# Kernel optimization log

Measured on AMD Instinct MI355X. Metric: run time of the kernel, lower is better.

The kernel has to match this reference:

```python
import jax, jax.numpy as jnp
import numpy as np

C = 64
K = 16
DEPTH = 4            # int(sqrt(K))
N_NODES = K - 1      # 15 internal nodes per subspace tree
D = 512              # input feature dim, D // C = 8 per subspace
M = 512              # output dim (LUT rows)
N = 16384            # number of input rows


def _make_selection_matrix(C, depth=DEPTH):
    # row i within a subspace selects the transformed dim used at tree level of node i
    lvl = [0, 1, 1, 2, 2, 2, 2, 3, 3, 3, 3, 3, 3, 3, 3]
    S = np.zeros((C * N_NODES, C * depth), np.float32)
    for c in range(C):
        for i in range(N_NODES):
            S[c * N_NODES + i, c * depth + lvl[i]] = 1.0
    return S


def _make_bit_matrix(C, K=K):
    # per-subspace (K, K-1) matrix: leaf k gets +/-1 on the 4 nodes along its root-to-leaf path
    Bm = np.zeros((K, N_NODES), np.float32)
    for k in range(K):
        node = 0
        for l in range(DEPTH):
            bit = (k >> (DEPTH - 1 - l)) & 1
            Bm[k, node] = 1.0 if bit else -1.0
            node = 2 * node + 1 + bit  # children of node i are 2i+1 (left) and 2i+2 (right)
    Bfull = np.zeros((C * K, C * N_NODES), np.float32)
    for c in range(C):
        Bfull[c * K:(c + 1) * K, c * N_NODES:(c + 1) * N_NODES] = Bm
    return Bfull


def setup_inputs() -> dict:
    key = jax.random.key(0)
    k1, k2, k3, k4 = jax.random.split(key, 4)
    I = jax.random.normal(k1, (N, D), dtype=jnp.float32)
    A = jax.random.normal(k2, (C, D // C, DEPTH), dtype=jnp.float32) * (1.0 / np.sqrt(D // C))
    T = jax.random.normal(k3, (C * N_NODES,), dtype=jnp.float32) * 0.1
    L = jax.random.normal(k4, (M, C, K), dtype=jnp.float32)
    S = jnp.asarray(_make_selection_matrix(C))
    B = jnp.asarray(_make_bit_matrix(C))
    return {"I": I, "A": A, "T": T, "L": L, "S": S, "B": B}


def reference(I, A, T, L, S, B):
    C_, sub, depth = A.shape
    Kq = L.shape[-1]
    n = I.shape[0]
    # block-diagonal per-subspace projection: (n, D) -> (n, C*depth)
    Ir = I.T.reshape(C_, sub, n)                      # (C, sub, n)
    xt = jnp.einsum('csn,csd->cdn', Ir, A)            # (C, depth, n)
    xt = xt.reshape(C_ * depth, n)                    # (C*depth, n)
    # tree encoding: per-node activations, tanh relaxation, leaf scores
    h = S @ xt - T[:, None]                           # (C*15, n)
    b = (B @ jnp.tanh(h)).reshape(C_, Kq, n)          # (C, K, n)
    # straight-through hard one-hot encoding with softmax backward
    E_soft = jax.nn.softmax(b, axis=1)
    E_hard = jax.nn.one_hot(jnp.argmax(b, axis=1), Kq, axis=1, dtype=b.dtype)
    E = E_hard + E_soft - jax.lax.stop_gradient(E_soft)  # (C, K, n)
    # LUT decode: out[n, m] = sum_c L[m, c, enc(n, c)]
    out = jnp.einsum('mck,ckn->nm', L, E)
    return out
```

## Files before the change

kernel.cpp:

```cpp
#include <hip/hip_runtime.h>
#include <hip/hip_fp16.h>
#include <math.h>

#define CC 64
#define KK 16
#define NNODES 15
#define DD 512
#define MM 512
#define NN 16384

typedef _Float16 half8 __attribute__((ext_vector_type(8)));
typedef float f32x4 __attribute__((ext_vector_type(4)));
typedef unsigned long long u64;

__device__ __forceinline__ float xla_tanhf(float x) {
    const float kMax = 7.90531110763549805f;
    bool tiny = fabsf(x) < 0.0004f;
    float xc = fminf(fmaxf(x, -kMax), kMax);
    float x2 = __fmul_rn(xc, xc);
    float p = __fmaf_rn(x2, -2.76076847742355e-16f, 2.00018790482477e-13f);
    p = __fmaf_rn(x2, p, -8.60467152213735e-11f);
    p = __fmaf_rn(x2, p, 5.12229709037114e-08f);
    p = __fmaf_rn(x2, p, 1.48572235717979e-05f);
    p = __fmaf_rn(x2, p, 6.37261928875436e-04f);
    p = __fmaf_rn(x2, p, 4.89352455891786e-03f);
    p = __fmul_rn(xc, p);
    float q = __fmaf_rn(x2, 1.19825839466702e-06f, 1.18534705686654e-04f);
    q = __fmaf_rn(x2, q, 2.26843463243900e-03f);
    q = __fmaf_rn(x2, q, 4.89352518554385e-03f);
    return tiny ? x : __fdiv_rn(p, q);
}

__global__ __launch_bounds__(256) void pack_bfrag(const float* __restrict__ L,
                                                  uint4* __restrict__ Bpk) {
    const int t    = blockIdx.x * 256 + threadIdx.x;
    const int lane = t & 63;
    const int mtg  = (t >> 6) & 31;
    const int ks   = t >> 11;
    const int kbase = ks * 32 + ((lane >> 4) << 3);
    const int c     = kbase >> 4;
    const int slot0 = kbase & 15;
    const int m     = (mtg << 4) + (lane & 15);

    const float* src = L + ((size_t)m * CC + c) * KK + slot0;
    float4 v0 = ((const float4*)src)[0];
    float4 v1 = ((const float4*)src)[1];
    union { half8 h; uint4 u; } pk;
    pk.h[0] = (_Float16)v0.x; pk.h[1] = (_Float16)v0.y;
    pk.h[2] = (_Float16)v0.z; pk.h[3] = (_Float16)v0.w;
    pk.h[4] = (_Float16)v1.x; pk.h[5] = (_Float16)v1.y;
    pk.h[6] = (_Float16)v1.z; pk.h[7] = (_Float16)v1.w;
    Bpk[t] = pk.u;
}

__global__ __launch_bounds__(256, 4) void encode_kernel(const float* __restrict__ I,
                                                        const float* __restrict__ A,
                                                        const float* __restrict__ T,
                                                        unsigned* __restrict__ codesG) {
    __shared__ float sA[32 * 64];
    __shared__ float sT[CC * NNODES];

    const int tid = threadIdx.x;
    for (int i = tid; i < CC * 32; i += 256) sA[(i & 31) * 64 + (i >> 5)] = A[i];
    for (int i = tid; i < CC * NNODES; i += 256) sT[i] = T[i];
    __syncthreads();

    const int lane = tid & 63;
    const int c    = lane;
    const int w    = ((blockIdx.x & 3) << 2) + (tid >> 6);
    const int tile = blockIdx.x >> 2;
    const int n0   = tile * 64;

    float a_[32];
#pragma unroll
    for (int i = 0; i < 32; ++i) a_[i] = sA[i * 64 + c];
    float tt[NNODES];
#pragma unroll
    for (int i = 0; i < NNODES; ++i) tt[i] = sT[c * NNODES + i];

    const int lvl[NNODES] = {0, 1, 1, 2, 2, 2, 2, 3, 3, 3, 3, 3, 3, 3, 3};
    unsigned codeWord = 0;
#pragma unroll 2
    for (int rr = 0; rr < 4; ++rr) {
        const int rl = (rr << 4) + w;
        const float* Ij = I + (size_t)(n0 + rl) * DD + c * 8;
        float4 v0 = ((const float4*)Ij)[0];
        float4 v1 = ((const float4*)Ij)[1];
        float iv[8] = {v0.x, v0.y, v0.z, v0.w, v1.x, v1.y, v1.z, v1.w};

        float t[4] = {0.f, 0.f, 0.f, 0.f};
#pragma unroll
        for (int s = 0; s < 8; ++s) {
            float v = iv[s];
#pragma unroll
            for (int d = 0; d < 4; ++d)
                t[d] = __fmaf_rn(v, a_[(s << 2) + d], t[d]);
        }

        float th[NNODES];
#pragma unroll
        for (int i = 0; i < NNODES; ++i) {
            float h = __fsub_rn(t[lvl[i]], tt[i]);
            th[i] = xla_tanhf(h);
        }

        int best = 0;
        float bestv = -3.0e38f;
#pragma unroll
        for (int k = 0; k < KK; ++k) {
            int node = 0;
            float s = 0.f;
#pragma unroll
            for (int l = 0; l < 4; ++l) {
                int bit = (k >> (3 - l)) & 1;
                s = __fadd_rn(s, bit ? th[node] : -th[node]);
                node = 2 * node + 1 + bit;
            }
            if (s > bestv) { bestv = s; best = k; }
        }
        codeWord |= ((unsigned)best) << (rr << 3);
    }
    codesG[(size_t)tile * 1024 + (w << 6) + c] = codeWord;
}

__global__ __launch_bounds__(256, 4) void decode_kernel(const unsigned* __restrict__ codesG,
                                                        const uint4* __restrict__ Bpk,
                                                        float* __restrict__ out) {
    __shared__ unsigned sCodes[16 * 68];

    const int tid  = threadIdx.x;
    const int tile = blockIdx.x >> 2;
    const int mq   = blockIdx.x & 3;
    const int n0   = tile * 64;

#pragma unroll
    for (int kk = 0; kk < 4; ++kk) {
        int i = tid + (kk << 8);
        sCodes[(i >> 6) * 68 + (i & 63)] = codesG[(size_t)tile * 1024 + i];
    }
    __syncthreads();

    const int w    = tid >> 6;
    const int lane = tid & 63;
    const int wn   = w;
    const int r15  = lane & 15;
    const int sb   = ((lane >> 4) & 1) << 3;
    const int chi  = lane >> 5;
    const int wnsh = wn << 3;

    f32x4 acc[8];
#pragma unroll
    for (int mt = 0; mt < 8; ++mt) acc[mt] = (f32x4){0.f, 0.f, 0.f, 0.f};

    const uint4* Bp = Bpk + (size_t)(mq << 3) * 64 + lane;
    const unsigned* codeRow = sCodes + r15 * 68;

    uint4 bX[8], bY[8];
#pragma unroll
    for (int mt = 0; mt < 8; ++mt) bX[mt] = Bp[mt * 64];
    unsigned cwA = codeRow[chi];
    unsigned cwB;

    for (int ks = 0; ks < 32; ks += 2) {
#pragma unroll
        for (int mt = 0; mt < 8; ++mt) bY[mt] = Bp[((ks + 1) * 32 + mt) * 64];
        cwB = codeRow[(ks + 1) * 2 + chi];

        {
            unsigned ud  = ((cwA >> wnsh) & 255u) - (unsigned)sb;
            unsigned ud2 = ud - 4u;
            u64 lo = (ud  < 4u) ? (0x3C00ull << ((ud  & 3u) << 4)) : 0ull;
            u64 hi = (ud2 < 4u) ? (0x3C00ull << ((ud2 & 3u) << 4)) : 0ull;
            union { u64 q[2]; half8 h; } uu; uu.q[0] = lo; uu.q[1] = hi;
#pragma unroll
            for (int mt = 0; mt < 8; ++mt) {
                union { uint4 u; half8 h; } bb; bb.u = bX[mt];
                acc[mt] = __builtin_amdgcn_mfma_f32_16x16x32_f16(uu.h, bb.h, acc[mt], 0, 0, 0);
            }
        }

        if (ks + 2 < 32) {
#pragma unroll
            for (int mt = 0; mt < 8; ++mt) bX[mt] = Bp[((ks + 2) * 32 + mt) * 64];
            cwA = codeRow[(ks + 2) * 2 + chi];
        }

        {
            unsigned ud  = ((cwB >> wnsh) & 255u) - (unsigned)sb;
            unsigned ud2 = ud - 4u;
            u64 lo = (ud  < 4u) ? (0x3C00ull << ((ud  & 3u) << 4)) : 0ull;
            u64 hi = (ud2 < 4u) ? (0x3C00ull << ((ud2 & 3u) << 4)) : 0ull;
            union { u64 q[2]; half8 h; } uu; uu.q[0] = lo; uu.q[1] = hi;
#pragma unroll
            for (int mt = 0; mt < 8; ++mt) {
                union { uint4 u; half8 h; } bb; bb.u = bY[mt];
                acc[mt] = __builtin_amdgcn_mfma_f32_16x16x32_f16(uu.h, bb.h, acc[mt], 0, 0, 0);
            }
        }
    }

    const int rbase = (lane >> 4) << 2;
#pragma unroll
    for (int mt = 0; mt < 8; ++mt) {
#pragma unroll
        for (int r = 0; r < 4; ++r) {
            out[(size_t)(n0 + (wn << 4) + rbase + r) * MM + (mq << 7) + (mt << 4) + r15] = acc[mt][r];
        }
    }
}

extern "C" void kernel_launch(void* const* d_in, const int* in_sizes, int n_in,
                              void* d_out, int out_size, void* d_ws, size_t ws_size,
                              hipStream_t stream) {
    const float* I = (const float*)d_in[0];
    const float* A = (const float*)d_in[1];
    const float* T = (const float*)d_in[2];
    const float* L = (const float*)d_in[3];

    uint4* Bpk = (uint4*)d_ws;
    unsigned* codesG = (unsigned*)((char*)d_ws + (1 << 20));
    float* out = (float*)d_out;

    hipLaunchKernelGGL(pack_bfrag, dim3(256), dim3(256), 0, stream, L, Bpk);
    hipLaunchKernelGGL(encode_kernel, dim3(1024), dim3(256), 0, stream, I, A, T, codesG);
    hipLaunchKernelGGL(decode_kernel, dim3(1024), dim3(256), 0, stream, codesG, Bpk, out);
}
```

Measured before the change: 139.5 us.

## Tile decode 128x128 with LDS double-buffered LUT fragments via global_load_lds

Reshapes the decode GEMM so each block covers 128 rows by 128 output columns with a 2x2 wave layout. The packed LUT fragments are staged into shared memory with async global-to-LDS loads and double-buffered, so all waves in a block share them instead of each wave fetching its own. This cuts redundant global/L2 traffic for the B operand. In exchange it adds a block-wide barrier per k-step and uses more accumulator registers, which lowers occupancy.

```diff
diff --git a/kernel.cpp b/kernel.cpp
--- a/kernel.cpp
+++ b/kernel.cpp
@@ -123,88 +123,101 @@
     codesG[(size_t)tile * 1024 + (w << 6) + c] = codeWord;
 }
 
-__global__ __launch_bounds__(256, 4) void decode_kernel(const unsigned* __restrict__ codesG,
+__global__ __launch_bounds__(256, 2) void decode_kernel(const unsigned* __restrict__ codesG,
                                                         const uint4* __restrict__ Bpk,
                                                         float* __restrict__ out) {
-    __shared__ unsigned sCodes[16 * 68];
-
-    const int tid  = threadIdx.x;
-    const int tile = blockIdx.x >> 2;
-    const int mq   = blockIdx.x & 3;
-    const int n0   = tile * 64;
-
-#pragma unroll
-    for (int kk = 0; kk < 4; ++kk) {
-        int i = tid + (kk << 8);
-        sCodes[(i >> 6) * 68 + (i & 63)] = codesG[(size_t)tile * 1024 + i];
-    }
-    __syncthreads();
+    __shared__ __align__(16) unsigned char sB[2][8192];
+    __shared__ unsigned sCodes[2][16 * 68];
+
+    const int tid = threadIdx.x;
+    const int bn  = blockIdx.x >> 2;
+    const int bm  = blockIdx.x & 3;
+    const int n0  = bn << 7;
+    const int m0  = bm << 7;
+
+#pragma unroll
+    for (int k = 0; k < 8; ++k) {
+        int i = tid + (k << 8);
+        sCodes[i >> 10][((i >> 6) & 15) * 68 + (i & 63)] = codesG[((size_t)bn << 11) + i];
+    }
 
     const int w    = tid >> 6;
     const int lane = tid & 63;
-    const int wn   = w;
+    const int wn   = w >> 1;
+    const int wm   = w & 1;
     const int r15  = lane & 15;
     const int sb   = ((lane >> 4) & 1) << 3;
     const int chi  = lane >> 5;
-    const int wnsh = wn << 3;
-
-    f32x4 acc[8];
-#pragma unroll
-    for (int mt = 0; mt < 8; ++mt) acc[mt] = (f32x4){0.f, 0.f, 0.f, 0.f};
-
-    const uint4* Bp = Bpk + (size_t)(mq << 3) * 64 + lane;
-    const unsigned* codeRow = sCodes + r15 * 68;
-
-    uint4 bX[8], bY[8];
-#pragma unroll
-    for (int mt = 0; mt < 8; ++mt) bX[mt] = Bp[mt * 64];
-    unsigned cwA = codeRow[chi];
-    unsigned cwB;
-
-    for (int ks = 0; ks < 32; ks += 2) {
-#pragma unroll
-        for (int mt = 0; mt < 8; ++mt) bY[mt] = Bp[((ks + 1) * 32 + mt) * 64];
-        cwB = codeRow[(ks + 1) * 2 + chi];
-
-        {
-            unsigned ud  = ((cwA >> wnsh) & 255u) - (unsigned)sb;
+
+    const uint4* gA = Bpk + ((bm << 3) + w) * 64 + lane;
+    const uint4* gB = gA + 4 * 64;
+
+    __builtin_amdgcn_global_load_lds(
+        (const __attribute__((address_space(1))) void*)gA,
+        (__attribute__((address_space(3))) void*)&sB[0][w << 10], 16, 0, 0);
+    __builtin_amdgcn_global_load_lds(
+        (const __attribute__((address_space(1))) void*)gB,
+        (__attribute__((address_space(3))) void*)&sB[0][(w + 4) << 10], 16, 0, 0);
+    gA += 2048; gB += 2048;
+    __syncthreads();
+
+    f32x4 acc[4][4];
+#pragma unroll
+    for (int nt = 0; nt < 4; ++nt)
+#pragma unroll
+        for (int mt = 0; mt < 4; ++mt)
+            acc[nt][mt] = (f32x4){0.f, 0.f, 0.f, 0.f};
+
+    const unsigned* codeRow = &sCodes[wn][r15 * 68];
+    const int bvoff = (wm << 2) << 10;
+
+#pragma unroll 2
+    for (int ks = 0; ks < 32; ++ks) {
+        const int cur = ks & 1;
+        if (ks < 31) {
+            __builtin_amdgcn_global_load_lds(
+                (const __attribute__((address_space(1))) void*)gA,
+                (__attribute__((address_space(3))) void*)&sB[cur ^ 1][w << 10], 16, 0, 0);
+            __builtin_amdgcn_global_load_lds(
+                (const __attribute__((address_space(1))) void*)gB,
+                (__attribute__((address_space(3))) void*)&sB[cur ^ 1][(w + 4) << 10], 16, 0, 0);
+            gA += 2048; gB += 2048;
+        }
+
+        const unsigned cw = codeRow[(ks << 1) + chi];
+
+        uint4 b[4];
+#pragma unroll
+        for (int j = 0; j < 4; ++j)
+            b[j] = *(const uint4*)&sB[cur][bvoff + (j << 10) + (lane << 4)];
+
+#pragma unroll
+        for (int nt = 0; nt < 4; ++nt) {
+            unsigned ud  = ((cw >> (nt << 3)) & 255u) - (unsigned)sb;
             unsigned ud2 = ud - 4u;
             u64 lo = (ud  < 4u) ? (0x3C00ull << ((ud  & 3u) << 4)) : 0ull;
             u64 hi = (ud2 < 4u) ? (0x3C00ull << ((ud2 & 3u) << 4)) : 0ull;
             union { u64 q[2]; half8 h; } uu; uu.q[0] = lo; uu.q[1] = hi;
 #pragma unroll
-            for (int mt = 0; mt < 8; ++mt) {
-                union { uint4 u; half8 h; } bb; bb.u = bX[mt];
-                acc[mt] = __builtin_amdgcn_mfma_f32_16x16x32_f16(uu.h, bb.h, acc[mt], 0, 0, 0);
+            for (int mt = 0; mt < 4; ++mt) {
+                union { uint4 u; half8 h; } bb; bb.u = b[mt];
+                acc[nt][mt] = __builtin_amdgcn_mfma_f32_16x16x32_f16(uu.h, bb.h, acc[nt][mt], 0, 0, 0);
             }
         }
 
-        if (ks + 2 < 32) {
-#pragma unroll
-            for (int mt = 0; mt < 8; ++mt) bX[mt] = Bp[((ks + 2) * 32 + mt) * 64];
-            cwA = codeRow[(ks + 2) * 2 + chi];
-        }
-
-        {
-            unsigned ud  = ((cwB >> wnsh) & 255u) - (unsigned)sb;
-            unsigned ud2 = ud - 4u;
-            u64 lo = (ud  < 4u) ? (0x3C00ull << ((ud  & 3u) << 4)) : 0ull;
-            u64 hi = (ud2 < 4u) ? (0x3C00ull << ((ud2 & 3u) << 4)) : 0ull;
-            union { u64 q[2]; half8 h; } uu; uu.q[0] = lo; uu.q[1] = hi;
-#pragma unroll
-            for (int mt = 0; mt < 8; ++mt) {
-                union { uint4 u; half8 h; } bb; bb.u = bY[mt];
-                acc[mt] = __builtin_amdgcn_mfma_f32_16x16x32_f16(uu.h, bb.h, acc[mt], 0, 0, 0);
-            }
-        }
+        __syncthreads();
     }
 
     const int rbase = (lane >> 4) << 2;
 #pragma unroll
-    for (int mt = 0; mt < 8; ++mt) {
+    for (int nt = 0; nt < 4; ++nt) {
 #pragma unroll
         for (int r = 0; r < 4; ++r) {
-            out[(size_t)(n0 + (wn << 4) + rbase + r) * MM + (mq << 7) + (mt << 4) + r15] = acc[mt][r];
+            float* o = out + (size_t)(n0 + ((wn << 2) + nt) * 16 + rbase + r) * MM
+                           + m0 + (wm << 6) + r15;
+#pragma unroll
+            for (int mt = 0; mt < 4; ++mt)
+                o[mt << 4] = acc[nt][mt][r];
         }
     }
 }
@@ -223,5 +236,5 @@
 
     hipLaunchKernelGGL(pack_bfrag, dim3(256), dim3(256), 0, stream, L, Bpk);
     hipLaunchKernelGGL(encode_kernel, dim3(1024), dim3(256), 0, stream, I, A, T, codesG);
-    hipLaunchKernelGGL(decode_kernel, dim3(1024), dim3(256), 0, stream, codesG, Bpk, out);
-}
+    hipLaunchKernelGGL(decode_kernel, dim3(512), dim3(256), 0, stream, codesG, Bpk, out);
+}
```

Result: faster. 128.9 us (-7.6%).
